# Kernel optimization log

Measured on AMD Instinct MI355X. Metric: run time of the kernel, lower is better.

The kernel has to match this reference:

```python
import jax, jax.numpy as jnp
import numpy as np

D = 768
N_HEADS = 12
HEAD_DIM = 64
INNER = N_HEADS * HEAD_DIM
SCALE = HEAD_DIM ** -0.5
EPS = 1e-5


def setup_inputs() -> dict:
    key = jax.random.key(0)
    ks = jax.random.split(key, 7)
    s = 0.02
    return {
        "x": jax.random.normal(ks[0], (2, 2048, D), dtype=jnp.float32),
        "Wq": jax.random.normal(ks[1], (D, INNER), dtype=jnp.float32) * s,
        "Wk": jax.random.normal(ks[2], (D, INNER), dtype=jnp.float32) * s,
        "Wv": jax.random.normal(ks[3], (D, INNER), dtype=jnp.float32) * s,
        "Wo": jax.random.normal(ks[4], (INNER, D), dtype=jnp.float32) * s,
        "bo": jnp.zeros((D,), dtype=jnp.float32),
        "gamma": jnp.ones((D,), dtype=jnp.float32),
        "beta": jnp.zeros((D,), dtype=jnp.float32),
    }


def _layernorm(x, gamma, beta):
    mu = jnp.mean(x, axis=-1, keepdims=True)
    var = jnp.var(x, axis=-1, keepdims=True)
    return (x - mu) * jax.lax.rsqrt(var + EPS) * gamma + beta


def reference(x, Wq, Wk, Wv, Wo, bo, gamma, beta):
    b, n, _ = x.shape
    h = _layernorm(x, gamma, beta)
    # project and split heads: [b, n, inner] -> [b, h, n, d]
    def split(t):
        return t.reshape(b, n, N_HEADS, HEAD_DIM).transpose(0, 2, 1, 3)
    Q = split(h @ Wq)
    K = split(h @ Wk)
    V = split(h @ Wv)
    # NOTE: module applies softmax first, THEN multiplies probs by scale
    attn = jnp.einsum('bhid,bhjd->bhij', Q, K)
    attn = jax.nn.softmax(attn, axis=-1) * SCALE
    vals = jnp.einsum('bhij,bhjd->bhid', attn, V)
    vals = vals.transpose(0, 2, 1, 3).reshape(b, n, INNER)
    out = vals @ Wo + bo
    return x + out
```

## Files before the change

### kernel.cpp

```cpp
#include <hip/hip_runtime.h>
#include <stdint.h>

typedef __bf16 bf16;
typedef __bf16 bf16x8 __attribute__((ext_vector_type(8)));
typedef float  f32x4  __attribute__((ext_vector_type(4)));
typedef unsigned short u16x4 __attribute__((ext_vector_type(4)));
typedef unsigned int   u32x4v __attribute__((ext_vector_type(4)));

#define SEQ   2048
#define DM    768
#define NH    12
#define HD    64
#define ATT_SCALE 0.125f
#define LOG2E 1.44269504f
#define LN_EPS 1e-5f

__device__ __forceinline__ void gload16(const void* g, void* l) {
  __builtin_amdgcn_global_load_lds((const __attribute__((address_space(1))) void*)g,
                                   (__attribute__((address_space(3))) void*)l,
                                   16, 0, 0);
}

__global__ __launch_bounds__(256) void prep_kernel(
    const float* __restrict__ x, const float* __restrict__ gamma,
    const float* __restrict__ beta, bf16* __restrict__ h,
    const float* __restrict__ Wq, const float* __restrict__ Wk,
    const float* __restrict__ Wv, const float* __restrict__ Wo,
    bf16* __restrict__ Wqkvt, bf16* __restrict__ Wot)
{
  __shared__ float smem[32*33];
  int bid = blockIdx.x, t = threadIdx.x;
  if (bid < 4096) {
    const float* xr = x + (size_t)bid*DM;
    float v0 = xr[t], v1 = xr[t+256], v2 = xr[t+512];
    float s = v0+v1+v2;
    float q = v0*v0+v1*v1+v2*v2;
    #pragma unroll
    for (int m=32;m>=1;m>>=1){ s += __shfl_xor(s,m,64); q += __shfl_xor(q,m,64); }
    float* rs = smem; float* rq = smem+8;
    int w = t>>6;
    if ((t&63)==0){ rs[w]=s; rq[w]=q; }
    __syncthreads();
    float S = rs[0]+rs[1]+rs[2]+rs[3];
    float Q = rq[0]+rq[1]+rq[2]+rq[3];
    float mean = S*(1.0f/DM);
    float var  = Q*(1.0f/DM) - mean*mean;
    float rstd = rsqrtf(var + LN_EPS);
    bf16* hr = h + (size_t)bid*DM;
    hr[t]     = (bf16)((v0-mean)*rstd*gamma[t]     + beta[t]);
    hr[t+256] = (bf16)((v1-mean)*rstd*gamma[t+256] + beta[t+256]);
    hr[t+512] = (bf16)((v2-mean)*rstd*gamma[t+512] + beta[t+512]);
  } else {
    int tb = bid - 4096;
    int z = tb/576, rem = tb%576;
    int r0 = (rem/24)*32, c0 = (rem%24)*32;
    int tx = t&31, ty = t>>5;
    float (*tile)[33] = (float(*)[33])smem;
    const float* src = (z==0)?Wq:(z==1)?Wk:(z==2)?Wv:Wo;
    #pragma unroll
    for (int i=ty;i<32;i+=8) tile[i][tx] = src[(size_t)(r0+i)*DM + c0+tx];
    __syncthreads();
    bf16* dst = (z<3) ? (Wqkvt + (size_t)z*DM*DM) : Wot;
    #pragma unroll
    for (int i=ty;i<32;i+=8) dst[(size_t)(c0+i)*DM + r0+tx] = (bf16)tile[tx][i];
  }
}

template<int BM, int BN, int WM, int WN, int EPI>
__global__ __launch_bounds__(256) void gemm_bt(
    const bf16* __restrict__ A, const bf16* __restrict__ Bt, int K,
    bf16* __restrict__ qk, bf16* __restrict__ vt,
    float* __restrict__ out, const float* __restrict__ bo, const float* __restrict__ xres)
{
  constexpr int MF = BM/(WM*16);
  constexpr int NF = BN/(WN*16);
  constexpr int GL = BM/64 + BN/64;
  __shared__ bf16 As[3][BM][32];
  __shared__ bf16 Bs[3][BN][32];
  int tid = threadIdx.x, w = tid>>6, la = tid&63;
  int bn = blockIdx.x, bm = blockIdx.y;
  int wm = w / WN, wn = w % WN;
  int g = la>>4, li = la&15;
  int sr = la>>2, sc = (la&3)*8;
  f32x4 acc[MF][NF] = {};
  const int KT = K/32;

  auto stage = [&](int kt, int bb) {
    int k0 = kt*32;
    #pragma unroll
    for (int i=0;i<BM/64;i++){ int r0 = i*64 + w*16;
      gload16(A + ((size_t)(bm*BM + r0 + sr))*K + k0 + sc, &As[bb][r0][0]); }
    #pragma unroll
    for (int i=0;i<BN/64;i++){ int r0 = i*64 + w*16;
      gload16(Bt + ((size_t)(bn*BN + r0 + sr))*K + k0 + sc, &Bs[bb][r0][0]); }
  };

  stage(0,0); stage(1,1);
  asm volatile("s_waitcnt vmcnt(%0)" :: "n"(GL) : "memory");
  __builtin_amdgcn_s_barrier();
  __builtin_amdgcn_sched_barrier(0);

  for (int kt=0; kt<KT; ++kt) {
    int bb = kt%3;
    if (kt+2 < KT) stage(kt+2, (kt+2)%3);
    bf16x8 af[MF], bfr[NF];
    #pragma unroll
    for (int i=0;i<MF;i++) af[i]  = *(const bf16x8*)&As[bb][wm*(BM/WM)+i*16+li][g*8];
    #pragma unroll
    for (int j=0;j<NF;j++) bfr[j] = *(const bf16x8*)&Bs[bb][wn*(BN/WN)+j*16+li][g*8];
    __builtin_amdgcn_s_setprio(1);
    #pragma unroll
    for (int i=0;i<MF;i++)
      #pragma unroll
      for (int j=0;j<NF;j++)
        acc[i][j] = __builtin_amdgcn_mfma_f32_16x16x32_bf16(af[i], bfr[j], acc[i][j], 0,0,0);
    __builtin_amdgcn_s_setprio(0);
    if (kt+1 < KT) {
      if (kt+2 < KT) asm volatile("s_waitcnt vmcnt(%0)" :: "n"(GL) : "memory");
      else           asm volatile("s_waitcnt vmcnt(0)" ::: "memory");
      __builtin_amdgcn_s_barrier();
      __builtin_amdgcn_sched_barrier(0);
    }
  }

  #pragma unroll
  for (int i=0;i<MF;i++){
    int row0 = bm*BM + wm*(BM/WM) + i*16 + g*4;
    #pragma unroll
    for (int j=0;j<NF;j++){
      int col = bn*BN + wn*(BN/WN) + j*16 + li;
      if (EPI==0){
        if (col < 1536) {
          float qs = (col < 768) ? LOG2E : 1.0f;
          #pragma unroll
          for (int r=0;r<4;r++) qk[(size_t)(row0+r)*1536 + col] = (bf16)(acc[i][j][r]*qs);
        } else {
          int cv = col - 1536; int hh = cv>>6, dd = cv&63;
          int b_ = row0>>11,  n0 = row0&2047;
          u16x4 u;
          #pragma unroll
          for (int r=0;r<4;r++){ bf16 bv = (bf16)acc[i][j][r];
            u[r] = __builtin_bit_cast(unsigned short, bv); }
          *reinterpret_cast<u16x4*>(vt + ((size_t)((b_*NH+hh)*HD+dd))*SEQ + n0) = u;
        }
      } else {
        float bb2 = bo[col];
        #pragma unroll
        for (int r=0;r<4;r++){ size_t idx = (size_t)(row0+r)*DM + col;
          out[idx] = acc[i][j][r] + bb2 + xres[idx]; }
      }
    }
  }
}

__global__ __launch_bounds__(128) void attn_kernel(
    const bf16* __restrict__ QK, const bf16* __restrict__ Vt, bf16* __restrict__ vals)
{
  __shared__ bf16 Ks[3][64][64];
  __shared__ bf16 Vs[3][64][64];
  int tid=threadIdx.x, w=tid>>6, la=tid&63;
  int id = blockIdx.x;
  int xcd = id & 7, idx = id >> 3;
  int bh  = xcd*3 + (idx>>5);
  int qt  = idx & 31;
  int b = bh/NH, hh = bh%NH;
  int g=la>>4, li=la&15;
  int lr=la>>3;
  int lx=li&7;
  int lcs=((la&7)^lr)*8;
  size_t qrow0=(size_t)b*SEQ + qt*64;

  bf16x8 qf[2][2];
  #pragma unroll
  for (int qh=0;qh<2;qh++){
    const bf16* qp = QK + (qrow0 + w*32 + qh*16 + li)*1536 + hh*64;
    qf[0][qh] = *(const bf16x8*)(qp + g*8);
    qf[1][qh] = *(const bf16x8*)(qp + 32 + g*8);
  }

  bf16x8 onef;
  {
    unsigned int one2 = 0x3F803F80u;
    u32x4v oc = {one2, one2, one2, one2};
    onef = __builtin_bit_cast(bf16x8, oc);
  }

  const bf16* Kbase = QK + (size_t)b*SEQ*1536 + 768 + hh*64;
  const bf16* Vbase = Vt + (size_t)(b*NH+hh)*HD*SEQ;

  auto stage = [&](int tt, int bb) {
    int j0 = tt*64;
    #pragma unroll
    for (int i=0;i<4;i++){ int c=i*2+w;
      gload16(Kbase + (size_t)(j0 + c*8 + lr)*1536 + lcs, &Ks[bb][c*8][0]);
      gload16(Vbase + (size_t)(c*8 + lr)*SEQ + j0 + lcs,  &Vs[bb][c*8][0]); }
  };

  stage(0,0); stage(1,1);
  asm volatile("s_waitcnt vmcnt(8)" ::: "memory");
  __builtin_amdgcn_s_barrier();
  __builtin_amdgcn_sched_barrier(0);

  f32x4 o[2][4] = {};
  f32x4 ol[2] = {};

  for (int t=0;t<32;t++){
    int bb = t%3;
    if (t+2 < 32) stage(t+2, (t+2)%3);
    f32x4 s[2][4] = {};
    #pragma unroll
    for (int kk=0;kk<2;kk++){
      bf16x8 kf[4];
      #pragma unroll
      for (int nf=0;nf<4;nf++){
        int row = nf*16+li;
        kf[nf] = *(const bf16x8*)((const char*)&Ks[bb][0][0] + row*128 + (((kk*4+g)^lx)<<4));
      }
      __builtin_amdgcn_s_setprio(1);
      #pragma unroll
      for (int nf=0;nf<4;nf++){
        s[0][nf] = __builtin_amdgcn_mfma_f32_16x16x32_bf16(kf[nf], qf[kk][0], s[0][nf], 0,0,0);
        s[1][nf] = __builtin_amdgcn_mfma_f32_16x16x32_bf16(kf[nf], qf[kk][1], s[1][nf], 0,0,0);
      }
      __builtin_amdgcn_s_setprio(0);
    }
    bf16x8 pa[2][2];
    #pragma unroll
    for (int qh=0;qh<2;qh++){
      float p[4][4];
      #pragma unroll
      for (int nf=0;nf<4;nf++)
        #pragma unroll
        for (int r=0;r<4;r++)
          p[nf][r] = __builtin_amdgcn_exp2f(s[qh][nf][r]);
      #pragma unroll
      for (int ks=0;ks<2;ks++){
        unsigned int c00,c01,c10,c11;
        asm("v_cvt_pk_bf16_f32 %0, %1, %2" : "=v"(c00) : "v"(p[2*ks  ][0]), "v"(p[2*ks  ][1]));
        asm("v_cvt_pk_bf16_f32 %0, %1, %2" : "=v"(c01) : "v"(p[2*ks  ][2]), "v"(p[2*ks  ][3]));
        asm("v_cvt_pk_bf16_f32 %0, %1, %2" : "=v"(c10) : "v"(p[2*ks+1][0]), "v"(p[2*ks+1][1]));
        asm("v_cvt_pk_bf16_f32 %0, %1, %2" : "=v"(c11) : "v"(p[2*ks+1][2]), "v"(p[2*ks+1][3]));
        asm("v_permlane32_swap_b32 %0, %1" : "+v"(c00), "+v"(c10));
        asm("v_permlane32_swap_b32 %0, %1" : "+v"(c01), "+v"(c11));
        asm("v_permlane16_swap_b32 %0, %1" : "+v"(c00), "+v"(c10));
        asm("v_permlane16_swap_b32 %0, %1" : "+v"(c01), "+v"(c11));
        u32x4v cc = {c00, c01, c10, c11};
        pa[qh][ks] = __builtin_bit_cast(bf16x8, cc);
      }
    }
    #pragma unroll
    for (int ks=0;ks<2;ks++){
      bf16x8 vb[4];
      #pragma unroll
      for (int df=0;df<4;df++){
        int row = df*16+li;
        vb[df] = *(const bf16x8*)((const char*)&Vs[bb][0][0] + row*128 + (((ks*4+g)^lx)<<4));
      }
      __builtin_amdgcn_s_setprio(1);
      #pragma unroll
      for (int qh=0;qh<2;qh++){
        #pragma unroll
        for (int df=0;df<4;df++)
          o[qh][df] = __builtin_amdgcn_mfma_f32_16x16x32_bf16(vb[df], pa[qh][ks], o[qh][df], 0,0,0);
        ol[qh] = __builtin_amdgcn_mfma_f32_16x16x32_bf16(onef, pa[qh][ks], ol[qh], 0,0,0);
      }
      __builtin_amdgcn_s_setprio(0);
    }
    if (t+1 < 32) {
      if (t+2 < 32) asm volatile("s_waitcnt vmcnt(8)" ::: "memory");
      else          asm volatile("s_waitcnt vmcnt(0)" ::: "memory");
      __builtin_amdgcn_s_barrier();
      __builtin_amdgcn_sched_barrier(0);
    }
  }
  #pragma unroll
  for (int qh=0;qh<2;qh++){
    float fac = ATT_SCALE / ol[qh][0];
    bf16* vrow = vals + (qrow0 + w*32 + qh*16 + li)*DM + hh*64;
    #pragma unroll
    for (int df=0;df<4;df++){
      u16x4 u;
      #pragma unroll
      for (int r=0;r<4;r++){
        bf16 bv = (bf16)(o[qh][df][r] * fac);
        u[r] = __builtin_bit_cast(unsigned short, bv);
      }
      *reinterpret_cast<u16x4*>(vrow + df*16 + g*4) = u;
    }
  }
}

extern "C" void kernel_launch(void* const* d_in, const int* in_sizes, int n_in,
                              void* d_out, int out_size, void* d_ws, size_t ws_size,
                              hipStream_t stream)
{
  const float* x     = (const float*)d_in[0];
  const float* Wq    = (const float*)d_in[1];
  const float* Wk    = (const float*)d_in[2];
  const float* Wv    = (const float*)d_in[3];
  const float* Wo    = (const float*)d_in[4];
  const float* bo    = (const float*)d_in[5];
  const float* gamma = (const float*)d_in[6];
  const float* beta  = (const float*)d_in[7];
  float* out = (float*)d_out;
  char* ws = (char*)d_ws;

  bf16* h     = (bf16*)(ws + 0);
  bf16* vals  = (bf16*)(ws + 0);
  bf16* Wqkvt = (bf16*)(ws + 6291456);
  bf16* Wot   = (bf16*)(ws + 9830400);
  bf16* QKb   = (bf16*)(ws + 11010048);
  bf16* Vt    = (bf16*)(ws + 23592960);
  (void)ws_size; (void)in_sizes; (void)n_in; (void)out_size;

  prep_kernel<<<dim3(6400), dim3(256), 0, stream>>>(
      x, gamma, beta, h, Wq, Wk, Wv, Wo, Wqkvt, Wot);
  gemm_bt<128,128,2,2,0><<<dim3(18,32), dim3(256), 0, stream>>>(
      h, Wqkvt, DM, QKb, Vt, nullptr, nullptr, nullptr);
  attn_kernel<<<dim3(768), dim3(128), 0, stream>>>(QKb, Vt, vals);
  gemm_bt<64,64,2,2,1><<<dim3(12,64), dim3(256), 0, stream>>>(
      vals, Wot, DM, nullptr, nullptr, out, bo, x);
}
```

Baseline: 114.0 us.

## Split attention KV range across two blocks and add a combine kernel

Each attention block now handles half of the key/value sequence, doubling the grid from 768 to 1536 blocks so the GPU has more resident work. Unnormalized partial outputs go to bf16 scratch, reusing the output buffer, and row sums go to workspace. A new reduce kernel adds the two halves and applies the scale divided by the summed normalizer. In exchange, the K/V pipeline drops from triple to double buffering with a full vmcnt(0) wait each step, which shortens prefetch lookahead. The change also adds an extra launch, extra global traffic for the partials, and bf16 rounding of the partial sums.

```diff
diff --git a/kernel.cpp b/kernel.cpp
--- a/kernel.cpp
+++ b/kernel.cpp
@@ -154,21 +154,25 @@
 }
 
 __global__ __launch_bounds__(128) void attn_kernel(
-    const bf16* __restrict__ QK, const bf16* __restrict__ Vt, bf16* __restrict__ vals)
-{
-  __shared__ bf16 Ks[3][64][64];
-  __shared__ bf16 Vs[3][64][64];
+    const bf16* __restrict__ QK, const bf16* __restrict__ Vt,
+    bf16* __restrict__ Opart, float* __restrict__ lpart)
+{
+  __shared__ bf16 Ks[2][64][64];
+  __shared__ bf16 Vs[2][64][64];
   int tid=threadIdx.x, w=tid>>6, la=tid&63;
   int id = blockIdx.x;
   int xcd = id & 7, idx = id >> 3;
-  int bh  = xcd*3 + (idx>>5);
-  int qt  = idx & 31;
+  int bh  = xcd*3 + idx/64;
+  int rem = idx & 63;
+  int qt  = rem >> 1;
+  int kvh = rem & 1;
   int b = bh/NH, hh = bh%NH;
   int g=la>>4, li=la&15;
   int lr=la>>3;
   int lx=li&7;
   int lcs=((la&7)^lr)*8;
   size_t qrow0=(size_t)b*SEQ + qt*64;
+  int kv0 = kvh*1024;
 
   bf16x8 qf[2][2];
   #pragma unroll
@@ -189,24 +193,24 @@
   const bf16* Vbase = Vt + (size_t)(b*NH+hh)*HD*SEQ;
 
   auto stage = [&](int tt, int bb) {
-    int j0 = tt*64;
+    int j0 = kv0 + tt*64;
     #pragma unroll
     for (int i=0;i<4;i++){ int c=i*2+w;
       gload16(Kbase + (size_t)(j0 + c*8 + lr)*1536 + lcs, &Ks[bb][c*8][0]);
       gload16(Vbase + (size_t)(c*8 + lr)*SEQ + j0 + lcs,  &Vs[bb][c*8][0]); }
   };
 
-  stage(0,0); stage(1,1);
-  asm volatile("s_waitcnt vmcnt(8)" ::: "memory");
+  stage(0,0);
+  asm volatile("s_waitcnt vmcnt(0)" ::: "memory");
   __builtin_amdgcn_s_barrier();
   __builtin_amdgcn_sched_barrier(0);
 
   f32x4 o[2][4] = {};
   f32x4 ol[2] = {};
 
-  for (int t=0;t<32;t++){
-    int bb = t%3;
-    if (t+2 < 32) stage(t+2, (t+2)%3);
+  for (int t=0;t<16;t++){
+    int bb = t&1;
+    if (t+1 < 16) stage(t+1, bb^1);
     f32x4 s[2][4] = {};
     #pragma unroll
     for (int kk=0;kk<2;kk++){
@@ -266,28 +270,46 @@
       }
       __builtin_amdgcn_s_setprio(0);
     }
-    if (t+1 < 32) {
-      if (t+2 < 32) asm volatile("s_waitcnt vmcnt(8)" ::: "memory");
-      else          asm volatile("s_waitcnt vmcnt(0)" ::: "memory");
+    if (t+1 < 16) {
+      asm volatile("s_waitcnt vmcnt(0)" ::: "memory");
       __builtin_amdgcn_s_barrier();
       __builtin_amdgcn_sched_barrier(0);
     }
   }
+  bf16* ob = Opart + (size_t)kvh*4096*DM;
   #pragma unroll
   for (int qh=0;qh<2;qh++){
-    float fac = ATT_SCALE / ol[qh][0];
-    bf16* vrow = vals + (qrow0 + w*32 + qh*16 + li)*DM + hh*64;
+    size_t row = qrow0 + w*32 + qh*16 + li;
     #pragma unroll
     for (int df=0;df<4;df++){
       u16x4 u;
       #pragma unroll
       for (int r=0;r<4;r++){
-        bf16 bv = (bf16)(o[qh][df][r] * fac);
+        bf16 bv = (bf16)o[qh][df][r];
         u[r] = __builtin_bit_cast(unsigned short, bv);
       }
-      *reinterpret_cast<u16x4*>(vrow + df*16 + g*4) = u;
-    }
-  }
+      *reinterpret_cast<u16x4*>(ob + row*DM + hh*64 + df*16 + g*4) = u;
+    }
+    if (g==0) lpart[(size_t)kvh*24*SEQ + (size_t)bh*SEQ + qt*64 + w*32 + qh*16 + li] = ol[qh][0];
+  }
+}
+
+__global__ __launch_bounds__(256) void reduce_kernel(
+    const bf16* __restrict__ Op, const float* __restrict__ lp, bf16* __restrict__ vals)
+{
+  int gid = blockIdx.x*256 + threadIdx.x;
+  int r = gid/96, cv = gid - r*96;
+  int c0 = cv*8;
+  int b = r>>11, q = r&2047, h = c0>>6;
+  size_t li = (size_t)(b*NH + h)*SEQ + q;
+  float l = lp[li] + lp[(size_t)24*SEQ + li];
+  float fac = ATT_SCALE / l;
+  bf16x8 a = *(const bf16x8*)(Op + (size_t)r*DM + c0);
+  bf16x8 bb = *(const bf16x8*)(Op + (size_t)4096*DM + (size_t)r*DM + c0);
+  bf16x8 o;
+  #pragma unroll
+  for (int i=0;i<8;i++) o[i] = (bf16)(((float)a[i] + (float)bb[i]) * fac);
+  *(bf16x8*)(vals + (size_t)r*DM + c0) = o;
 }
 
 extern "C" void kernel_launch(void* const* d_in, const int* in_sizes, int n_in,
@@ -311,13 +333,16 @@
   bf16* Wot   = (bf16*)(ws + 9830400);
   bf16* QKb   = (bf16*)(ws + 11010048);
   bf16* Vt    = (bf16*)(ws + 23592960);
+  bf16*  Opart = (bf16*)d_out;
+  float* lpart = (float*)(ws + 6291456);
   (void)ws_size; (void)in_sizes; (void)n_in; (void)out_size;
 
   prep_kernel<<<dim3(6400), dim3(256), 0, stream>>>(
       x, gamma, beta, h, Wq, Wk, Wv, Wo, Wqkvt, Wot);
   gemm_bt<128,128,2,2,0><<<dim3(18,32), dim3(256), 0, stream>>>(
       h, Wqkvt, DM, QKb, Vt, nullptr, nullptr, nullptr);
-  attn_kernel<<<dim3(768), dim3(128), 0, stream>>>(QKb, Vt, vals);
+  attn_kernel<<<dim3(1536), dim3(128), 0, stream>>>(QKb, Vt, Opart, lpart);
+  reduce_kernel<<<dim3(1536), dim3(256), 0, stream>>>(Opart, lpart, vals);
   gemm_bt<64,64,2,2,1><<<dim3(12,64), dim3(256), 0, stream>>>(
       vals, Wot, DM, nullptr, nullptr, out, bo, x);
 }
```

Measured after the change: 116.1 us. Within noise of the previous version (+1.9%).
